# Kernel optimization log

Hardware: AMD Instinct MI355X
Metric: run time of the kernel (lower is better)

## Reference

```python
import jax, jax.numpy as jnp
import numpy as np

MUL0, MUL1, SCALARS_OUT = 16, 16, 128
L0, L1 = MUL0, MUL1 * 3            # 16, 48
PATH_NUMEL = MUL0 * MUL1 * SCALARS_OUT  # 32768 per path, two paths
EPS = 1e-5
# e3nn normalization: irrep_normalization='component' -> alpha = dim(ir_out) = 1;
# path_normalization='element' -> divide by sum over paths to same output of mul1*mul2 = 256+256 = 512.
PATH_COEFF = 1.0 / np.sqrt(512.0)
CG_110 = 1.0 / np.sqrt(3.0)  # wigner_3j(1,1,0)[i,j] = delta_ij/sqrt(3) (unit Frobenius norm)


def layer_norm(x, g, b):
    mu = jnp.mean(x, axis=-1, keepdims=True)
    var = jnp.mean(jnp.square(x - mu), axis=-1, keepdims=True)
    return (x - mu) * jax.lax.rsqrt(var + EPS) * g + b


def ff_block(x, g, b, w1, w2, b2):
    # LayerNorm -> Linear(no bias) -> SiLU -> Linear(bias); residual=False in both uses
    h = jax.nn.silu(layer_norm(x, g, b) @ w1)
    return h @ w2 + b2


def setup_inputs() -> dict:
    key = jax.random.key(0)
    ks = jax.random.split(key, 8)
    N = 2048
    return {
        "x": jax.random.normal(ks[0], (N, L0 + L1), dtype=jnp.float32),
        "we_ln_g": jnp.ones((L0,), jnp.float32),
        "we_ln_b": jnp.zeros((L0,), jnp.float32),
        "we_w1": jax.random.normal(ks[1], (L0, 4 * L0), jnp.float32) / np.sqrt(L0),
        "we_w2": jax.random.normal(ks[2], (4 * L0, 2 * PATH_NUMEL), jnp.float32) / np.sqrt(4 * L0),
        "we_b2": jnp.zeros((2 * PATH_NUMEL,), jnp.float32),
        "om_ln_g": jnp.ones((SCALARS_OUT,), jnp.float32),
        "om_ln_b": jnp.zeros((SCALARS_OUT,), jnp.float32),
        "om_w1": jax.random.normal(ks[3], (SCALARS_OUT, 4 * SCALARS_OUT), jnp.float32) / np.sqrt(SCALARS_OUT),
        "om_w2": jax.random.normal(ks[4], (4 * SCALARS_OUT, 1), jnp.float32) / np.sqrt(4 * SCALARS_OUT),
        "om_b2": jnp.zeros((1,), jnp.float32),
    }


def reference(x, we_ln_g, we_ln_b, we_w1, we_w2, we_b2,
              om_ln_g, om_ln_b, om_w1, om_w2, om_b2):
    N = x.shape[0]
    feats = x[:, :L0]                       # [N, 16] scalars (0e)
    x1 = x[:, L0:].reshape(N, MUL1, 3)      # [N, 16, 3] vectors (1o)

    # per-sample tensor-product weights (shared_weights=False)
    w = ff_block(feats, we_ln_g, we_ln_b, we_w1, we_w2, we_b2)  # [N, 65536]
    w0 = w[:, :PATH_NUMEL].reshape(N, MUL0, MUL0, SCALARS_OUT)
    w1 = w[:, PATH_NUMEL:].reshape(N, MUL1, MUL1, SCALARS_OUT)

    # path 0: 0e x 0e -> 0e  (uvw)
    o0 = jnp.einsum('nu,nv,nuvw->nw', feats, feats, w0)
    # path 1: 1o x 1o -> 0e  (uvw, CG = delta_ij/sqrt(3))
    o1 = jnp.einsum('nui,nvi,nuvw->nw', x1, x1, w1) * CG_110
    tp_out = PATH_COEFF * (o0 + o1)          # [N, 128]

    return ff_block(tp_out, om_ln_g, om_ln_b, om_w1, om_w2, om_b2)  # [N, 1]
```

## Files before the change

### kernel.cpp

```cpp
#include <hip/hip_runtime.h>
#include <hip/hip_bf16.h>
#include <cstdint>

#define EPS 1e-5f
#define PATH_COEFF 0.04419417382415922f
#define CG110     0.5773502691896258f

typedef __bf16 v8bf __attribute__((ext_vector_type(8)));
typedef float  v4f  __attribute__((ext_vector_type(4)));
typedef _Float16 v4h __attribute__((ext_vector_type(4)));

static __device__ __forceinline__ unsigned short f2bf(float x){
    unsigned int u = __builtin_bit_cast(unsigned int, x);
    u += 0x7fffu + ((u >> 16) & 1u);
    return (unsigned short)(u >> 16);
}
static __device__ __forceinline__ unsigned short f2h(float x){
    return __builtin_bit_cast(unsigned short, (_Float16)x);
}

__global__ __launch_bounds__(256)
void k_pre(const float* __restrict__ w2, const float* __restrict__ b2,
           unsigned short* __restrict__ Vt2,
           const float* __restrict__ om_w1, unsigned short* __restrict__ w1t,
           const float* __restrict__ x, const float* __restrict__ lng,
           const float* __restrict__ lnb, const float* __restrict__ we_w1,
           unsigned short* __restrict__ Q2, float* __restrict__ Ht, int N)
{
    __shared__ __align__(16) unsigned short tile[32][128];
    int b = blockIdx.x;
    int t = threadIdx.x;

    if (b < 260){
        int k    = b >> 2;
        int slab = b & 3;
        const float* srcbase = (k < 64) ? (w2 + (size_t)k * 65536) : b2;
        for (int chunk = 0; chunk < 4; ++chunk){
            int pbase = slab*128 + chunk*32;
            #pragma unroll
            for (int i = 0; i < 4; ++i){
                int g = t + 256*i;
                int ploc = g >> 5, c4 = g & 31;
                const float4 v = *(const float4*)(srcbase + (size_t)(pbase + ploc)*128 + c4*4);
                unsigned int w0 = (unsigned)f2bf(v.x) | ((unsigned)f2bf(v.y) << 16);
                unsigned int w1 = (unsigned)f2bf(v.z) | ((unsigned)f2bf(v.w) << 16);
                *(uint2*)&tile[ploc][c4*4] = make_uint2(w0, w1);
            }
            __syncthreads();
            int w = t & 127, h = t >> 7;
            int ps = slab*4 + chunk;
            unsigned int words[8];
            #pragma unroll
            for (int g2 = 0; g2 < 8; ++g2)
                words[g2] = (unsigned)tile[h*16 + g2*2][w] | ((unsigned)tile[h*16 + g2*2 + 1][w] << 16);
            unsigned short* dq0 = Vt2 + (((size_t)(k*16 + ps)*4 + 2*h    )*128 + w)*8;
            unsigned short* dq1 = Vt2 + (((size_t)(k*16 + ps)*4 + 2*h + 1)*128 + w)*8;
            *(uint4*)dq0 = make_uint4(words[0], words[1], words[2], words[3]);
            *(uint4*)dq1 = make_uint4(words[4], words[5], words[6], words[7]);
            __syncthreads();
        }
    } else if (b < 264){
        int j0 = (b - 260) * 128;
        for (int chunk = 0; chunk < 4; ++chunk){
            #pragma unroll
            for (int i = 0; i < 4; ++i){
                int g = t + 256*i;
                int wloc = g >> 5, c4 = g & 31;
                int w = chunk*32 + wloc;
                const float4 v = *(const float4*)(om_w1 + (size_t)w*512 + j0 + c4*4);
                unsigned int a = (unsigned)f2bf(v.x) | ((unsigned)f2bf(v.y) << 16);
                unsigned int bb = (unsigned)f2bf(v.z) | ((unsigned)f2bf(v.w) << 16);
                *(uint2*)&tile[wloc][c4*4] = make_uint2(a, bb);
            }
            __syncthreads();
            int jl = t & 127, h = t >> 7;
            unsigned int words[8];
            #pragma unroll
            for (int g2 = 0; g2 < 8; ++g2)
                words[g2] = (unsigned)tile[h*16 + g2*2][jl] | ((unsigned)tile[h*16 + g2*2 + 1][jl] << 16);
            unsigned short* dst = w1t + (size_t)(j0 + jl)*128 + chunk*32 + h*16;
            *(uint4*)dst       = make_uint4(words[0], words[1], words[2], words[3]);
            *(uint4*)(dst + 8) = make_uint4(words[4], words[5], words[6], words[7]);
            __syncthreads();
        }
    } else {
        int wv = t >> 6, lane = t & 63;
        int row = (b - 264)*4 + wv;
        const float* xr = x + (size_t)row * 64;
        float f[16]; float mu = 0.f;
        #pragma unroll
        for (int u = 0; u < 16; ++u){ f[u] = xr[u]; mu += f[u]; }
        mu *= (1.f/16.f);
        float var = 0.f;
        #pragma unroll
        for (int u = 0; u < 16; ++u){ float d = f[u] - mu; var += d*d; }
        var *= (1.f/16.f);
        float inv = rsqrtf(var + EPS);
        float lnf[16];
        #pragma unroll
        for (int u = 0; u < 16; ++u) lnf[u] = (f[u]-mu)*inv*lng[u] + lnb[u];
        float h1 = 0.f;
        #pragma unroll
        for (int u = 0; u < 16; ++u) h1 += lnf[u] * we_w1[u*64 + lane];
        float h = h1 / (1.f + expf(-h1));
        Ht[(size_t)lane * N + row] = h;
        if (lane == 0) Ht[(size_t)64 * N + row] = 1.f;

        union { unsigned short qs[8]; uint4 v; } qu;
        #pragma unroll
        for (int j = 0; j < 8; ++j){
            int p = lane*8 + j;
            float q;
            if (p < 256){
                int u = p >> 4, v = p & 15;
                q = PATH_COEFF * f[u] * f[v];
            } else {
                int pp = p - 256;
                int u = pp >> 4, v = pp & 15;
                const float* ya = xr + 16 + u*3;
                const float* yb = xr + 16 + v*3;
                q = (PATH_COEFF * CG110) * (ya[0]*yb[0] + ya[1]*yb[1] + ya[2]*yb[2]);
            }
            qu.qs[j] = f2bf(q);
        }
        int rb = row >> 6, r64 = row & 63;
        int ps = lane >> 2, quad4 = lane & 3;
        *(uint4*)(Q2 + (((size_t)(rb*16 + ps)*4 + quad4)*64 + r64)*8) = qu.v;
    }
}

__global__ __launch_bounds__(256, 2)
void k_main(const unsigned short* __restrict__ Q2, const unsigned short* __restrict__ Vt2,
            const float* __restrict__ Ht, unsigned short* __restrict__ partial, int N)
{
    __shared__ __align__(16) unsigned short stile[4][64*72];
    int g = blockIdx.x & 7;
    int j = blockIdx.x >> 3;
    int kg, mb;
    if (j < 64){ mb = j >> 2; kg = g*4 + (j & 3); }
    else { if (g != 0) return; mb = j - 64; kg = 32; }

    int tid  = threadIdx.x;
    int lane = tid & 63, wv = tid >> 6;
    int r2 = wv >> 1, c2 = wv & 1;
    int quad = lane >> 4, l16 = lane & 15;
    int rowbase = mb*128 + r2*64;
    int rb = rowbase >> 6;
    int wbase = c2*64;

    int k0 = kg*2;
    int k1 = (kg == 32) ? 64 : k0 + 1;
    float sel = (kg == 32) ? 0.f : 1.f;

    const unsigned short* aroot  = Q2  + (size_t)rb*32768 + quad*512  + l16*8;
    const unsigned short* broot0 = Vt2 + (size_t)k0*65536 + quad*1024 + (wbase + l16)*8;
    const unsigned short* broot1 = Vt2 + (size_t)k1*65536 + quad*1024 + (wbase + l16)*8;

    v4f accA[4][4], accB[4][4];
    #pragma unroll
    for (int m=0;m<4;++m)
      #pragma unroll
      for (int n=0;n<4;++n)
        #pragma unroll
        for (int r=0;r<4;++r){ accA[m][n][r] = 0.f; accB[m][n][r] = 0.f; }

    #pragma unroll 2
    for (int ps = 0; ps < 16; ++ps){
        const unsigned short* ap  = aroot  + ps*2048;
        const unsigned short* bp0 = broot0 + ps*4096;
        const unsigned short* bp1 = broot1 + ps*4096;
        v8bf a[4], b0[4], b1[4];
        #pragma unroll
        for (int m=0;m<4;++m) a[m]  = *(const v8bf*)(ap  + m*128);
        #pragma unroll
        for (int n=0;n<4;++n) b0[n] = *(const v8bf*)(bp0 + n*128);
        #pragma unroll
        for (int n=0;n<4;++n) b1[n] = *(const v8bf*)(bp1 + n*128);
        #pragma unroll
        for (int m=0;m<4;++m)
          #pragma unroll
          for (int n=0;n<4;++n)
            accA[m][n] = __builtin_amdgcn_mfma_f32_16x16x32_bf16(a[m], b0[n], accA[m][n], 0, 0, 0);
        #pragma unroll
        for (int m=0;m<4;++m)
          #pragma unroll
          for (int n=0;n<4;++n)
            accB[m][n] = __builtin_amdgcn_mfma_f32_16x16x32_bf16(a[m], b1[n], accB[m][n], 0, 0, 0);
    }

    const float* hp0 = Ht + (size_t)k0*N + rowbase + quad*4;
    const float* hp1 = Ht + (size_t)k1*N + rowbase + quad*4;
    unsigned short* my = stile[wv];
    #pragma unroll
    for (int m=0;m<4;++m){
        v4f h0 = *(const v4f*)(hp0 + m*16);
        v4f h1 = *(const v4f*)(hp1 + m*16);
        #pragma unroll
        for (int n=0;n<4;++n)
          #pragma unroll
          for (int r=0;r<4;++r)
            my[(m*16 + quad*4 + r)*72 + n*16 + l16] =
                f2h(h0[r]*accA[m][n][r] + sel*h1[r]*accB[m][n][r]);
    }
    unsigned short* gp = partial + ((size_t)(mb*33 + kg))*16384
                                 + (size_t)(r2*64)*128 + wbase;
    #pragma unroll
    for (int i = 0; i < 8; ++i){
        int row = i*8 + (lane >> 3);
        int c16 = (lane & 7)*8;
        uint4 v = *(const uint4*)&my[row*72 + c16];
        *(uint4*)(gp + (size_t)row*128 + c16) = v;
    }
}

__global__ __launch_bounds__(128)
void k_red(const unsigned short* __restrict__ partial, const float* __restrict__ g,
           const float* __restrict__ b, unsigned short* __restrict__ lnf, int N)
{
    int t = threadIdx.x;
    int row = blockIdx.x * 8 + (t >> 4);
    int w8  = (t & 15) * 8;
    int mb  = row >> 7, rin = row & 127;

    const unsigned short* p0 = partial + (size_t)mb*33*16384 + (size_t)rin*128 + w8;

    float s[8];
    #pragma unroll
    for (int j = 0; j < 8; ++j) s[j] = 0.f;

    #pragma unroll 11
    for (int sl = 0; sl < 33; ++sl){
        uint4 raw = *(const uint4*)(p0 + (size_t)sl*16384);
        union { uint4 u; _Float16 h[8]; } cv; cv.u = raw;
        #pragma unroll
        for (int j = 0; j < 8; ++j) s[j] += (float)cv.h[j];
    }

    float sum = 0.f, sq = 0.f;
    #pragma unroll
    for (int j = 0; j < 8; ++j){ sum += s[j]; sq += s[j]*s[j]; }
    #pragma unroll
    for (int off = 8; off > 0; off >>= 1){
        sum += __shfl_xor(sum, off, 16);
        sq  += __shfl_xor(sq,  off, 16);
    }
    float mu  = sum * (1.f/128.f);
    float var = sq * (1.f/128.f) - mu*mu;
    float inv = rsqrtf(var + EPS);
    unsigned short o[8];
    #pragma unroll
    for (int j = 0; j < 8; ++j)
        o[j] = f2bf((s[j]-mu)*inv*g[w8+j] + b[w8+j]);
    *(uint4*)(lnf + (size_t)row*128 + w8) = *(uint4*)o;
}

__global__ __launch_bounds__(256)
void k_mlp2(const unsigned short* __restrict__ lnf, const unsigned short* __restrict__ w1t,
            const float* __restrict__ w2, const float* __restrict__ b2,
            float* __restrict__ out, int N)
{
    __shared__ float red2[4][32];
    int tid = threadIdx.x, lane = tid & 63, wv = tid >> 6;
    int quad = lane >> 4, l16 = lane & 15;
    int rowbase = blockIdx.x * 32;
    int jbase = wv * 128;

    v4f acc[2][8];
    #pragma unroll
    for (int m=0;m<2;++m)
      #pragma unroll
      for (int n=0;n<8;++n)
        #pragma unroll
        for (int r=0;r<4;++r) acc[m][n][r] = 0.f;

    #pragma unroll
    for (int ps = 0; ps < 4; ++ps){
        v8bf a[2], bb[8];
        #pragma unroll
        for (int m=0;m<2;++m)
            a[m]  = *(const v8bf*)(lnf + (size_t)(rowbase + m*16 + l16)*128 + ps*32 + quad*8);
        #pragma unroll
        for (int n=0;n<8;++n)
            bb[n] = *(const v8bf*)(w1t + (size_t)(jbase + n*16 + l16)*128 + ps*32 + quad*8);
        #pragma unroll
        for (int m=0;m<2;++m)
          #pragma unroll
          for (int n=0;n<8;++n)
            acc[m][n] = __builtin_amdgcn_mfma_f32_16x16x32_bf16(a[m], bb[n], acc[m][n], 0, 0, 0);
    }

    float w2v[8];
    #pragma unroll
    for (int n=0;n<8;++n) w2v[n] = w2[jbase + n*16 + l16];

    #pragma unroll
    for (int m=0;m<2;++m){
        #pragma unroll
        for (int r=0;r<4;++r){
            float s = 0.f;
            #pragma unroll
            for (int n=0;n<8;++n){
                float v = acc[m][n][r];
                s += (v / (1.f + expf(-v))) * w2v[n];
            }
            #pragma unroll
            for (int off=8; off>0; off>>=1) s += __shfl_xor(s, off, 16);
            if (l16 == 0) red2[wv][m*16 + quad*4 + r] = s;
        }
    }
    __syncthreads();
    if (tid < 32)
        out[rowbase + tid] = red2[0][tid] + red2[1][tid] + red2[2][tid] + red2[3][tid] + b2[0];
}

extern "C" void kernel_launch(void* const* d_in, const int* in_sizes, int n_in,
                              void* d_out, int out_size, void* d_ws, size_t ws_size,
                              hipStream_t stream)
{
    const float* x     = (const float*)d_in[0];
    const float* we_g  = (const float*)d_in[1];
    const float* we_b  = (const float*)d_in[2];
    const float* we_w1 = (const float*)d_in[3];
    const float* we_w2 = (const float*)d_in[4];
    const float* we_b2 = (const float*)d_in[5];
    const float* om_g  = (const float*)d_in[6];
    const float* om_b  = (const float*)d_in[7];
    const float* om_w1 = (const float*)d_in[8];
    const float* om_w2 = (const float*)d_in[9];
    const float* om_b2 = (const float*)d_in[10];

    int N  = in_sizes[0] / 64;

    char* ws = (char*)d_ws;
    size_t offV = 0;
    size_t szV  = (size_t)65*16*4*128*8*2;
    size_t offQ = offV + szV;
    size_t szQ  = (size_t)N*512*2;
    size_t offH = offQ + szQ;
    size_t szH  = (size_t)65*N*4;
    size_t offP = offH + szH;
    size_t szP  = (size_t)(N/128)*33*16384*2;
    size_t offL = offP + szP;
    size_t szL  = (size_t)N*128*2;
    size_t offW = offL + szL;

    unsigned short* Vt2 = (unsigned short*)(ws + offV);
    unsigned short* Q2  = (unsigned short*)(ws + offQ);
    float* Ht           = (float*)(ws + offH);
    unsigned short* Par = (unsigned short*)(ws + offP);
    unsigned short* Lnf = (unsigned short*)(ws + offL);
    unsigned short* W1t = (unsigned short*)(ws + offW);
    float* out = (float*)d_out;

    hipLaunchKernelGGL(k_pre,  dim3(264 + N/4), dim3(256), 0, stream,
                       we_w2, we_b2, Vt2, om_w1, W1t, x, we_g, we_b, we_w1, Q2, Ht, N);
    hipLaunchKernelGGL(k_main, dim3(80*8),      dim3(256), 0, stream, Q2, Vt2, Ht, Par, N);
    hipLaunchKernelGGL(k_red,  dim3(N/8),       dim3(128), 0, stream, Par, om_g, om_b, Lnf, N);
    hipLaunchKernelGGL(k_mlp2, dim3(N/32),      dim3(256), 0, stream, Lnf, W1t, om_w2, om_b2, out, N);
}
```

Baseline: 135.7 us.

## Fuse partial reduction, LayerNorm and output MLP into one tail kernel; coalesce prep stores

Merges k_red and k_mlp2 into a single k_tail kernel. Each 128-thread block reduces 33 fp16 partial slabs for 16 rows, applies LayerNorm into shared memory, then runs the bf16 MFMA MLP with SiLU and the output projection. This removes one kernel launch and the global round trip of the normalized activations. It also stages the Q2 and Ht writes of k_pre through shared memory so they are stored as coalesced vectors instead of scattered per-lane stores. In exchange, each block now has to stream the W1 weights for only 16 rows, and the tail launches fewer, smaller blocks.

```diff
diff --git a/kernel.cpp b/kernel.cpp
--- a/kernel.cpp
+++ b/kernel.cpp
@@ -28,6 +28,8 @@
            unsigned short* __restrict__ Q2, float* __restrict__ Ht, int N)
 {
     __shared__ __align__(16) unsigned short tile[32][128];
+    __shared__ __align__(16) uint4 qtile[64][4];
+    __shared__ float htile[4][65];
     int b = blockIdx.x;
     int t = threadIdx.x;
 
@@ -85,7 +87,8 @@
         }
     } else {
         int wv = t >> 6, lane = t & 63;
-        int row = (b - 264)*4 + wv;
+        int row0 = (b - 264)*4;
+        int row  = row0 + wv;
         const float* xr = x + (size_t)row * 64;
         float f[16]; float mu = 0.f;
         #pragma unroll
@@ -103,8 +106,8 @@
         #pragma unroll
         for (int u = 0; u < 16; ++u) h1 += lnf[u] * we_w1[u*64 + lane];
         float h = h1 / (1.f + expf(-h1));
-        Ht[(size_t)lane * N + row] = h;
-        if (lane == 0) Ht[(size_t)64 * N + row] = 1.f;
+        htile[wv][lane] = h;
+        if (lane == 0) htile[wv][64] = 1.f;
 
         union { unsigned short qs[8]; uint4 v; } qu;
         #pragma unroll
@@ -123,9 +126,18 @@
             }
             qu.qs[j] = f2bf(q);
         }
-        int rb = row >> 6, r64 = row & 63;
-        int ps = lane >> 2, quad4 = lane & 3;
-        *(uint4*)(Q2 + (((size_t)(rb*16 + ps)*4 + quad4)*64 + r64)*8) = qu.v;
+        qtile[lane][wv] = qu.v;
+        __syncthreads();
+
+        int rb = row0 >> 6, r64base = row0 & 63;
+        {
+            int slot = t >> 2, rr = t & 3;
+            ((uint4*)Q2)[(size_t)rb*4096 + (size_t)slot*64 + r64base + rr] = qtile[slot][rr];
+        }
+        if (t < 65){
+            float4 hv = make_float4(htile[0][t], htile[1][t], htile[2][t], htile[3][t]);
+            *(float4*)(Ht + (size_t)t*N + row0) = hv;
+        }
     }
 }
 
@@ -214,103 +226,96 @@
 }
 
 __global__ __launch_bounds__(128)
-void k_red(const unsigned short* __restrict__ partial, const float* __restrict__ g,
-           const float* __restrict__ b, unsigned short* __restrict__ lnf, int N)
-{
-    int t = threadIdx.x;
-    int row = blockIdx.x * 8 + (t >> 4);
-    int w8  = (t & 15) * 8;
-    int mb  = row >> 7, rin = row & 127;
-
-    const unsigned short* p0 = partial + (size_t)mb*33*16384 + (size_t)rin*128 + w8;
-
-    float s[8];
-    #pragma unroll
-    for (int j = 0; j < 8; ++j) s[j] = 0.f;
-
-    #pragma unroll 11
-    for (int sl = 0; sl < 33; ++sl){
-        uint4 raw = *(const uint4*)(p0 + (size_t)sl*16384);
-        union { uint4 u; _Float16 h[8]; } cv; cv.u = raw;
-        #pragma unroll
-        for (int j = 0; j < 8; ++j) s[j] += (float)cv.h[j];
-    }
-
-    float sum = 0.f, sq = 0.f;
-    #pragma unroll
-    for (int j = 0; j < 8; ++j){ sum += s[j]; sq += s[j]*s[j]; }
-    #pragma unroll
-    for (int off = 8; off > 0; off >>= 1){
-        sum += __shfl_xor(sum, off, 16);
-        sq  += __shfl_xor(sq,  off, 16);
-    }
-    float mu  = sum * (1.f/128.f);
-    float var = sq * (1.f/128.f) - mu*mu;
-    float inv = rsqrtf(var + EPS);
-    unsigned short o[8];
-    #pragma unroll
-    for (int j = 0; j < 8; ++j)
-        o[j] = f2bf((s[j]-mu)*inv*g[w8+j] + b[w8+j]);
-    *(uint4*)(lnf + (size_t)row*128 + w8) = *(uint4*)o;
-}
-
-__global__ __launch_bounds__(256)
-void k_mlp2(const unsigned short* __restrict__ lnf, const unsigned short* __restrict__ w1t,
+void k_tail(const unsigned short* __restrict__ partial, const float* __restrict__ g,
+            const float* __restrict__ b, const unsigned short* __restrict__ w1t,
             const float* __restrict__ w2, const float* __restrict__ b2,
             float* __restrict__ out, int N)
 {
-    __shared__ float red2[4][32];
-    int tid = threadIdx.x, lane = tid & 63, wv = tid >> 6;
+    __shared__ __align__(16) unsigned short lnf_lds[16][128];
+    __shared__ float red2[2][16];
+    int t = threadIdx.x;
+    int rowbase = blockIdx.x * 16;
+    int mb = rowbase >> 7;
+    const unsigned short* pbase = partial + (size_t)mb*33*16384;
+
+    #pragma unroll
+    for (int half = 0; half < 2; ++half){
+        int rl  = half*8 + (t >> 4);
+        int w8  = (t & 15) * 8;
+        int row = rowbase + rl;
+        int rin = row & 127;
+        const unsigned short* p0 = pbase + (size_t)rin*128 + w8;
+
+        float s[8];
+        #pragma unroll
+        for (int j2 = 0; j2 < 8; ++j2) s[j2] = 0.f;
+        #pragma unroll 11
+        for (int sl = 0; sl < 33; ++sl){
+            uint4 raw = *(const uint4*)(p0 + (size_t)sl*16384);
+            union { uint4 u; _Float16 h[8]; } cv; cv.u = raw;
+            #pragma unroll
+            for (int j2 = 0; j2 < 8; ++j2) s[j2] += (float)cv.h[j2];
+        }
+        float sum = 0.f, sq = 0.f;
+        #pragma unroll
+        for (int j2 = 0; j2 < 8; ++j2){ sum += s[j2]; sq += s[j2]*s[j2]; }
+        #pragma unroll
+        for (int off = 8; off > 0; off >>= 1){
+            sum += __shfl_xor(sum, off, 16);
+            sq  += __shfl_xor(sq,  off, 16);
+        }
+        float mu  = sum * (1.f/128.f);
+        float var = sq * (1.f/128.f) - mu*mu;
+        float inv = rsqrtf(var + EPS);
+        unsigned short o[8];
+        #pragma unroll
+        for (int j2 = 0; j2 < 8; ++j2)
+            o[j2] = f2bf((s[j2]-mu)*inv*g[w8+j2] + b[w8+j2]);
+        *(uint4*)&lnf_lds[rl][w8] = *(uint4*)o;
+    }
+    __syncthreads();
+
+    int lane = t & 63, wv = t >> 6;
     int quad = lane >> 4, l16 = lane & 15;
-    int rowbase = blockIdx.x * 32;
-    int jbase = wv * 128;
-
-    v4f acc[2][8];
-    #pragma unroll
-    for (int m=0;m<2;++m)
+    int jbase = wv * 256;
+
+    v4f acc[16];
+    #pragma unroll
+    for (int n=0;n<16;++n)
       #pragma unroll
-      for (int n=0;n<8;++n)
-        #pragma unroll
-        for (int r=0;r<4;++r) acc[m][n][r] = 0.f;
+      for (int r=0;r<4;++r) acc[n][r] = 0.f;
 
     #pragma unroll
     for (int ps = 0; ps < 4; ++ps){
-        v8bf a[2], bb[8];
-        #pragma unroll
-        for (int m=0;m<2;++m)
-            a[m]  = *(const v8bf*)(lnf + (size_t)(rowbase + m*16 + l16)*128 + ps*32 + quad*8);
-        #pragma unroll
-        for (int n=0;n<8;++n)
+        v8bf a = *(const v8bf*)&lnf_lds[l16][ps*32 + quad*8];
+        v8bf bb[16];
+        #pragma unroll
+        for (int n=0;n<16;++n)
             bb[n] = *(const v8bf*)(w1t + (size_t)(jbase + n*16 + l16)*128 + ps*32 + quad*8);
         #pragma unroll
-        for (int m=0;m<2;++m)
-          #pragma unroll
-          for (int n=0;n<8;++n)
-            acc[m][n] = __builtin_amdgcn_mfma_f32_16x16x32_bf16(a[m], bb[n], acc[m][n], 0, 0, 0);
-    }
-
-    float w2v[8];
-    #pragma unroll
-    for (int n=0;n<8;++n) w2v[n] = w2[jbase + n*16 + l16];
-
-    #pragma unroll
-    for (int m=0;m<2;++m){
-        #pragma unroll
-        for (int r=0;r<4;++r){
-            float s = 0.f;
-            #pragma unroll
-            for (int n=0;n<8;++n){
-                float v = acc[m][n][r];
-                s += (v / (1.f + expf(-v))) * w2v[n];
-            }
-            #pragma unroll
-            for (int off=8; off>0; off>>=1) s += __shfl_xor(s, off, 16);
-            if (l16 == 0) red2[wv][m*16 + quad*4 + r] = s;
-        }
+        for (int n=0;n<16;++n)
+            acc[n] = __builtin_amdgcn_mfma_f32_16x16x32_bf16(a, bb[n], acc[n], 0, 0, 0);
+    }
+
+    float w2v[16];
+    #pragma unroll
+    for (int n=0;n<16;++n) w2v[n] = w2[jbase + n*16 + l16];
+
+    #pragma unroll
+    for (int r=0;r<4;++r){
+        float s = 0.f;
+        #pragma unroll
+        for (int n=0;n<16;++n){
+            float v = acc[n][r];
+            s += (v / (1.f + expf(-v))) * w2v[n];
+        }
+        #pragma unroll
+        for (int off=8; off>0; off>>=1) s += __shfl_xor(s, off, 16);
+        if (l16 == 0) red2[wv][quad*4 + r] = s;
     }
     __syncthreads();
-    if (tid < 32)
-        out[rowbase + tid] = red2[0][tid] + red2[1][tid] + red2[2][tid] + red2[3][tid] + b2[0];
+    if (t < 16)
+        out[rowbase + t] = red2[0][t] + red2[1][t] + b2[0];
 }
 
 extern "C" void kernel_launch(void* const* d_in, const int* in_sizes, int n_in,
@@ -348,13 +353,12 @@
     unsigned short* Q2  = (unsigned short*)(ws + offQ);
     float* Ht           = (float*)(ws + offH);
     unsigned short* Par = (unsigned short*)(ws + offP);
-    unsigned short* Lnf = (unsigned short*)(ws + offL);
     unsigned short* W1t = (unsigned short*)(ws + offW);
     float* out = (float*)d_out;
 
     hipLaunchKernelGGL(k_pre,  dim3(264 + N/4), dim3(256), 0, stream,
                        we_w2, we_b2, Vt2, om_w1, W1t, x, we_g, we_b, we_w1, Q2, Ht, N);
     hipLaunchKernelGGL(k_main, dim3(80*8),      dim3(256), 0, stream, Q2, Vt2, Ht, Par, N);
-    hipLaunchKernelGGL(k_red,  dim3(N/8),       dim3(128), 0, stream, Par, om_g, om_b, Lnf, N);
-    hipLaunchKernelGGL(k_mlp2, dim3(N/32),      dim3(256), 0, stream, Lnf, W1t, om_w2, om_b2, out, N);
-}
+    hipLaunchKernelGGL(k_tail, dim3(N/16),      dim3(128), 0, stream,
+                       Par, om_g, om_b, W1t, om_w2, om_b2, out, N);
+}
```

New measurement: 135.0 us. Within noise of the previous version (-0.5%).
